# Optimization experiments

Measured on AMD Instinct MI355X. Metric: run time of the kernel, lower is better.

The kernel has to match this reference:

```python
import jax, jax.numpy as jnp
import numpy as np

EPS = 1e-8  # matches torch F.cosine_similarity eps


def setup_inputs() -> dict:
    key = jax.random.key(0)
    k1, k2, k3 = jax.random.split(key, 3)
    S, B, H = 16, 512, 2048
    OGLogits = jax.random.normal(k1, (B, H), dtype=jnp.float32)
    enhancedSamplesLogits = jax.random.normal(k2, (S, B, H), dtype=jnp.float32)
    W = jax.random.normal(k3, (H, H), dtype=jnp.float32) * (1.0 / np.sqrt(H))
    b = jnp.zeros((H,), dtype=jnp.float32)
    return {"OGLogits": OGLogits, "enhancedSamplesLogits": enhancedSamplesLogits, "W": W, "b": b}


def reference(OGLogits, enhancedSamplesLogits, W, b):
    # Original torch code builds the full (S*B, B) cosine-similarity matrix and
    # keeps only the diagonal via an eye mask; mathematically that equals the
    # per-pair cosine similarity cos(enhanced[s,b], OG[b]), computed directly here.
    e_norm = jnp.linalg.norm(enhancedSamplesLogits, axis=-1)          # (S, B)
    o_norm = jnp.linalg.norm(OGLogits, axis=-1)                       # (B,)
    dots = jnp.einsum('sbh,bh->sb', enhancedSamplesLogits, OGLogits)  # (S, B)
    sims = dots / jnp.maximum(e_norm * o_norm[None, :], EPS)          # (S, B)
    weighted = enhancedSamplesLogits * sims[..., None]                # (S, B, H)
    weightedRep = weighted.mean(axis=0)                               # (B, H)
    return weightedRep @ W.T + b                                      # (B, H)
```

## Files before the change

### kernel.cpp

```cpp
#include <hip/hip_runtime.h>

#define S_DIM 16
#define B_DIM 512
#define H_DIM 2048
#define EPS 1e-8f

typedef short bf16x8 __attribute__((ext_vector_type(8)));
typedef float f32x4 __attribute__((ext_vector_type(4)));

__device__ __forceinline__ unsigned short f2bf(float f) {
    union { float f; unsigned int u; } v; v.f = f;
    unsigned int u = v.u;
    unsigned int r = (u + 0x7fffu + ((u >> 16) & 1u)) >> 16;
    return (unsigned short)r;
}

__device__ __forceinline__ float dot4(const float4& a, const float4& b) {
    return a.x*b.x + a.y*b.y + a.z*b.z + a.w*b.w;
}

__global__ __launch_bounds__(512, 4) void simwrep_kernel(
    const float* __restrict__ OG, const float* __restrict__ E,
    const float* __restrict__ W, unsigned short* __restrict__ wrep,
    unsigned short* __restrict__ Wb) {
    const int b = blockIdx.x;
    const int t = threadIdx.x;
    const int lane = t & 63;
    const int wave = t >> 6;

    __shared__ float4 ogs[512];
    __shared__ float4 buf[8][512];
    __shared__ float red[8];

    const float4* og4 = (const float4*)(OG + (size_t)b * H_DIM);
    float4 o = og4[t];
    ogs[t] = o;
    float p = dot4(o, o);
    #pragma unroll
    for (int m = 32; m >= 1; m >>= 1) p += __shfl_xor(p, m, 64);
    if (lane == 0) red[wave] = p;
    __syncthreads();
    float og2 = 0.f;
    #pragma unroll
    for (int w = 0; w < 8; ++w) og2 += red[w];
    const float onorm = sqrtf(og2);

    const float4* e4a = (const float4*)(E + ((size_t)wave * B_DIM + b) * H_DIM);
    const float4* e4b = (const float4*)(E + ((size_t)(wave + 8) * B_DIM + b) * H_DIM);
    float4 ea[8], eb[8];
    #pragma unroll
    for (int i = 0; i < 8; ++i) {
        ea[i] = e4a[i * 64 + lane];
        eb[i] = e4b[i * 64 + lane];
    }
    float da = 0.f, na = 0.f, db = 0.f, nb = 0.f;
    #pragma unroll
    for (int i = 0; i < 8; ++i) {
        float4 og = ogs[i * 64 + lane];
        da += dot4(ea[i], og);
        na += dot4(ea[i], ea[i]);
        db += dot4(eb[i], og);
        nb += dot4(eb[i], eb[i]);
    }
    #pragma unroll
    for (int m = 32; m >= 1; m >>= 1) {
        da += __shfl_xor(da, m, 64);
        na += __shfl_xor(na, m, 64);
        db += __shfl_xor(db, m, 64);
        nb += __shfl_xor(nb, m, 64);
    }
    const float sima = da / fmaxf(sqrtf(na) * onorm, EPS);
    const float simb = db / fmaxf(sqrtf(nb) * onorm, EPS);

    #pragma unroll
    for (int i = 0; i < 8; ++i) {
        float4 v;
        v.x = ea[i].x * sima + eb[i].x * simb;
        v.y = ea[i].y * sima + eb[i].y * simb;
        v.z = ea[i].z * sima + eb[i].z * simb;
        v.w = ea[i].w * sima + eb[i].w * simb;
        buf[wave][i * 64 + lane] = v;
    }
    __syncthreads();

    float4 s = buf[0][t];
    #pragma unroll
    for (int w = 1; w < 8; ++w) {
        float4 v = buf[w][t];
        s.x += v.x; s.y += v.y; s.z += v.z; s.w += v.w;
    }
    const float sc = 1.f / (float)S_DIM;
    ushort4 ob;
    ob.x = f2bf(s.x * sc); ob.y = f2bf(s.y * sc);
    ob.z = f2bf(s.z * sc); ob.w = f2bf(s.w * sc);
    ((ushort4*)wrep)[(size_t)b * (H_DIM / 4) + t] = ob;

    const float4* w4 = (const float4*)W;
    #pragma unroll
    for (int j = 0; j < 4; ++j) {
        const size_t idx = (size_t)b * 2048 + j * 512 + t;
        float4 v = w4[idx];
        ushort4 c;
        c.x = f2bf(v.x); c.y = f2bf(v.y); c.z = f2bf(v.z); c.w = f2bf(v.w);
        ((ushort4*)Wb)[idx] = c;
    }
}

__global__ __launch_bounds__(256) void gemm_kernel(
    const unsigned short* __restrict__ A, const unsigned short* __restrict__ Wb,
    const float* __restrict__ bias, float* __restrict__ out) {
    const int n0 = blockIdx.x * 32;
    const int m0 = blockIdx.y * 64;

    __shared__ unsigned short As[2][64][72];
    __shared__ unsigned short Ws[2][32][72];

    const int t = threadIdx.x;
    const int lane = t & 63;
    const int wave = t >> 6;
    const int wm = (wave & 1) * 32;
    const int wn = (wave >> 1) * 16;

    const int lrA = t >> 2, lqA = t & 3;
    const int lrB = t >> 3, lqB = t & 7;

    const unsigned short* ap = A + (size_t)(m0 + lrA) * H_DIM + lqA * 16;
    const unsigned short* bp = Wb + (size_t)(n0 + lrB) * H_DIM + lqB * 8;

    f32x4 acc0 = {0.f, 0.f, 0.f, 0.f};
    f32x4 acc1 = {0.f, 0.f, 0.f, 0.f};

    const int row = lane & 15;
    const int q = lane >> 4;

    uint4 av0 = *(const uint4*)(ap);
    uint4 av1 = *(const uint4*)(ap + 8);
    uint4 bv  = *(const uint4*)(bp);
    *(uint4*)&As[0][lrA][lqA * 16]     = av0;
    *(uint4*)&As[0][lrA][lqA * 16 + 8] = av1;
    *(uint4*)&Ws[0][lrB][lqB * 8]      = bv;
    __syncthreads();

    for (int ki = 0; ki < 32; ++ki) {
        const int cur = ki & 1, nxt = cur ^ 1;
        if (ki + 1 < 32) {
            av0 = *(const uint4*)(ap + (ki + 1) * 64);
            av1 = *(const uint4*)(ap + (ki + 1) * 64 + 8);
            bv  = *(const uint4*)(bp + (ki + 1) * 64);
        }
        #pragma unroll
        for (int ks = 0; ks < 2; ++ks) {
            bf16x8 a0 = *(const bf16x8*)&As[cur][wm + row][ks * 32 + q * 8];
            bf16x8 a1 = *(const bf16x8*)&As[cur][wm + 16 + row][ks * 32 + q * 8];
            bf16x8 b0 = *(const bf16x8*)&Ws[cur][wn + row][ks * 32 + q * 8];
            acc0 = __builtin_amdgcn_mfma_f32_16x16x32_bf16(a0, b0, acc0, 0, 0, 0);
            acc1 = __builtin_amdgcn_mfma_f32_16x16x32_bf16(a1, b0, acc1, 0, 0, 0);
        }
        if (ki + 1 < 32) {
            *(uint4*)&As[nxt][lrA][lqA * 16]     = av0;
            *(uint4*)&As[nxt][lrA][lqA * 16 + 8] = av1;
            *(uint4*)&Ws[nxt][lrB][lqB * 8]      = bv;
        }
        __syncthreads();
    }

    const int col = lane & 15;
    const float bias0 = bias[n0 + wn + col];
    #pragma unroll
    for (int r = 0; r < 4; ++r) {
        const int mr = q * 4 + r;
        float* o0 = out + (size_t)(m0 + wm + mr) * H_DIM + n0 + wn;
        float* o1 = out + (size_t)(m0 + wm + 16 + mr) * H_DIM + n0 + wn;
        o0[col] = acc0[r] + bias0;
        o1[col] = acc1[r] + bias0;
    }
}

extern "C" void kernel_launch(void* const* d_in, const int* in_sizes, int n_in,
                              void* d_out, int out_size, void* d_ws, size_t ws_size,
                              hipStream_t stream) {
    const float* OG   = (const float*)d_in[0];
    const float* E    = (const float*)d_in[1];
    const float* W    = (const float*)d_in[2];
    const float* bias = (const float*)d_in[3];
    float* out = (float*)d_out;

    unsigned short* wrep = (unsigned short*)d_ws;
    unsigned short* Wb   = wrep + (size_t)B_DIM * H_DIM;

    simwrep_kernel<<<B_DIM, 512, 0, stream>>>(OG, E, W, wrep, Wb);
    gemm_kernel<<<dim3(H_DIM / 32, B_DIM / 64), 256, 0, stream>>>(wrep, Wb, bias, out);
}
```

Measured before the change: 126.3 us.

## Split similarity and weighted mean into separate kernels; use 32x32 MFMA tiles in GEMM

The fused per-batch kernel is split in two. One kernel computes the cosine similarity of each (s,b) row with one wave per row, and extra blocks in the same launch convert W to bf16. A second kernel re-reads E to form the weighted mean. The GEMM moves from a 64x32 tile built on 16x16x32 MFMAs to a 64x64 tile built on 32x32x16 MFMAs, which improves operand reuse and halves the grid. The price is reading E, about 64 MB, twice plus one extra kernel launch, in exchange for more parallelism in the similarity stage.

```diff
diff --git a/kernel.cpp b/kernel.cpp
--- a/kernel.cpp
+++ b/kernel.cpp
@@ -6,7 +6,7 @@
 #define EPS 1e-8f
 
 typedef short bf16x8 __attribute__((ext_vector_type(8)));
-typedef float f32x4 __attribute__((ext_vector_type(4)));
+typedef float f32x16 __attribute__((ext_vector_type(16)));
 
 __device__ __forceinline__ unsigned short f2bf(float f) {
     union { float f; unsigned int u; } v; v.f = f;
@@ -19,160 +19,138 @@
     return a.x*b.x + a.y*b.y + a.z*b.z + a.w*b.w;
 }
 
-__global__ __launch_bounds__(512, 4) void simwrep_kernel(
+__global__ __launch_bounds__(256) void sims_kernel(
     const float* __restrict__ OG, const float* __restrict__ E,
-    const float* __restrict__ W, unsigned short* __restrict__ wrep,
+    const float* __restrict__ W, float* __restrict__ sims,
     unsigned short* __restrict__ Wb) {
+    const int bid = blockIdx.x;
+    if (bid < (S_DIM * B_DIM / 4)) {
+        const int lane = threadIdx.x & 63;
+        const int r = bid * 4 + (threadIdx.x >> 6);
+        const int b = r & (B_DIM - 1);
+        const float4* e4  = (const float4*)E  + (size_t)r * (H_DIM / 4);
+        const float4* og4 = (const float4*)OG + (size_t)b * (H_DIM / 4);
+        float d = 0.f, n = 0.f, o = 0.f;
+        #pragma unroll
+        for (int i = 0; i < 8; ++i) {
+            float4 e = e4[i * 64 + lane];
+            float4 g = og4[i * 64 + lane];
+            d += dot4(e, g); n += dot4(e, e); o += dot4(g, g);
+        }
+        #pragma unroll
+        for (int m = 32; m >= 1; m >>= 1) {
+            d += __shfl_xor(d, m, 64);
+            n += __shfl_xor(n, m, 64);
+            o += __shfl_xor(o, m, 64);
+        }
+        if (lane == 0) sims[r] = d / fmaxf(sqrtf(n) * sqrtf(o), EPS);
+    } else {
+        const int wb = bid - (S_DIM * B_DIM / 4);
+        const int t = threadIdx.x;
+        const float4* w4 = (const float4*)W;
+        ushort4* wb4 = (ushort4*)Wb;
+        #pragma unroll
+        for (int j = 0; j < 8; ++j) {
+            const size_t idx = (size_t)wb * 2048 + j * 256 + t;
+            float4 v = w4[idx];
+            ushort4 c;
+            c.x = f2bf(v.x); c.y = f2bf(v.y); c.z = f2bf(v.z); c.w = f2bf(v.w);
+            wb4[idx] = c;
+        }
+    }
+}
+
+__global__ __launch_bounds__(512) void wmean_kernel(
+    const float* __restrict__ E, const float* __restrict__ sims,
+    unsigned short* __restrict__ wrep) {
     const int b = blockIdx.x;
     const int t = threadIdx.x;
-    const int lane = t & 63;
-    const int wave = t >> 6;
-
-    __shared__ float4 ogs[512];
-    __shared__ float4 buf[8][512];
-    __shared__ float red[8];
-
-    const float4* og4 = (const float4*)(OG + (size_t)b * H_DIM);
-    float4 o = og4[t];
-    ogs[t] = o;
-    float p = dot4(o, o);
+    __shared__ float sl[S_DIM];
+    const float4* e4 = (const float4*)E;
+    float4 ev[S_DIM];
     #pragma unroll
-    for (int m = 32; m >= 1; m >>= 1) p += __shfl_xor(p, m, 64);
-    if (lane == 0) red[wave] = p;
+    for (int s = 0; s < S_DIM; ++s)
+        ev[s] = e4[((size_t)s * B_DIM + b) * (H_DIM / 4) + t];
+    if (t < S_DIM) sl[t] = sims[t * B_DIM + b];
     __syncthreads();
-    float og2 = 0.f;
+    float x = 0.f, y = 0.f, z = 0.f, w = 0.f;
     #pragma unroll
-    for (int w = 0; w < 8; ++w) og2 += red[w];
-    const float onorm = sqrtf(og2);
-
-    const float4* e4a = (const float4*)(E + ((size_t)wave * B_DIM + b) * H_DIM);
-    const float4* e4b = (const float4*)(E + ((size_t)(wave + 8) * B_DIM + b) * H_DIM);
-    float4 ea[8], eb[8];
-    #pragma unroll
-    for (int i = 0; i < 8; ++i) {
-        ea[i] = e4a[i * 64 + lane];
-        eb[i] = e4b[i * 64 + lane];
-    }
-    float da = 0.f, na = 0.f, db = 0.f, nb = 0.f;
-    #pragma unroll
-    for (int i = 0; i < 8; ++i) {
-        float4 og = ogs[i * 64 + lane];
-        da += dot4(ea[i], og);
-        na += dot4(ea[i], ea[i]);
-        db += dot4(eb[i], og);
-        nb += dot4(eb[i], eb[i]);
-    }
-    #pragma unroll
-    for (int m = 32; m >= 1; m >>= 1) {
-        da += __shfl_xor(da, m, 64);
-        na += __shfl_xor(na, m, 64);
-        db += __shfl_xor(db, m, 64);
-        nb += __shfl_xor(nb, m, 64);
-    }
-    const float sima = da / fmaxf(sqrtf(na) * onorm, EPS);
-    const float simb = db / fmaxf(sqrtf(nb) * onorm, EPS);
-
-    #pragma unroll
-    for (int i = 0; i < 8; ++i) {
-        float4 v;
-        v.x = ea[i].x * sima + eb[i].x * simb;
-        v.y = ea[i].y * sima + eb[i].y * simb;
-        v.z = ea[i].z * sima + eb[i].z * simb;
-        v.w = ea[i].w * sima + eb[i].w * simb;
-        buf[wave][i * 64 + lane] = v;
-    }
-    __syncthreads();
-
-    float4 s = buf[0][t];
-    #pragma unroll
-    for (int w = 1; w < 8; ++w) {
-        float4 v = buf[w][t];
-        s.x += v.x; s.y += v.y; s.z += v.z; s.w += v.w;
+    for (int s = 0; s < S_DIM; ++s) {
+        const float sm = sl[s];
+        x += sm * ev[s].x; y += sm * ev[s].y;
+        z += sm * ev[s].z; w += sm * ev[s].w;
     }
     const float sc = 1.f / (float)S_DIM;
     ushort4 ob;
-    ob.x = f2bf(s.x * sc); ob.y = f2bf(s.y * sc);
-    ob.z = f2bf(s.z * sc); ob.w = f2bf(s.w * sc);
+    ob.x = f2bf(x * sc); ob.y = f2bf(y * sc);
+    ob.z = f2bf(z * sc); ob.w = f2bf(w * sc);
     ((ushort4*)wrep)[(size_t)b * (H_DIM / 4) + t] = ob;
-
-    const float4* w4 = (const float4*)W;
-    #pragma unroll
-    for (int j = 0; j < 4; ++j) {
-        const size_t idx = (size_t)b * 2048 + j * 512 + t;
-        float4 v = w4[idx];
-        ushort4 c;
-        c.x = f2bf(v.x); c.y = f2bf(v.y); c.z = f2bf(v.z); c.w = f2bf(v.w);
-        ((ushort4*)Wb)[idx] = c;
-    }
 }
 
 __global__ __launch_bounds__(256) void gemm_kernel(
     const unsigned short* __restrict__ A, const unsigned short* __restrict__ Wb,
     const float* __restrict__ bias, float* __restrict__ out) {
-    const int n0 = blockIdx.x * 32;
+    const int n0 = blockIdx.x * 64;
     const int m0 = blockIdx.y * 64;
 
     __shared__ unsigned short As[2][64][72];
-    __shared__ unsigned short Ws[2][32][72];
+    __shared__ unsigned short Bs[2][64][72];
 
     const int t = threadIdx.x;
     const int lane = t & 63;
     const int wave = t >> 6;
     const int wm = (wave & 1) * 32;
-    const int wn = (wave >> 1) * 16;
+    const int wn = (wave >> 1) * 32;
 
-    const int lrA = t >> 2, lqA = t & 3;
-    const int lrB = t >> 3, lqB = t & 7;
+    const int lr = t >> 2, lq = t & 3;
+    const unsigned short* ap = A  + (size_t)(m0 + lr) * H_DIM + lq * 16;
+    const unsigned short* bp = Wb + (size_t)(n0 + lr) * H_DIM + lq * 16;
 
-    const unsigned short* ap = A + (size_t)(m0 + lrA) * H_DIM + lqA * 16;
-    const unsigned short* bp = Wb + (size_t)(n0 + lrB) * H_DIM + lqB * 8;
+    f32x16 acc = {0.f,0.f,0.f,0.f,0.f,0.f,0.f,0.f,
+                  0.f,0.f,0.f,0.f,0.f,0.f,0.f,0.f};
 
-    f32x4 acc0 = {0.f, 0.f, 0.f, 0.f};
-    f32x4 acc1 = {0.f, 0.f, 0.f, 0.f};
+    const int row = lane & 31;
+    const int hi = lane >> 5;
 
-    const int row = lane & 15;
-    const int q = lane >> 4;
-
-    uint4 av0 = *(const uint4*)(ap);
-    uint4 av1 = *(const uint4*)(ap + 8);
-    uint4 bv  = *(const uint4*)(bp);
-    *(uint4*)&As[0][lrA][lqA * 16]     = av0;
-    *(uint4*)&As[0][lrA][lqA * 16 + 8] = av1;
-    *(uint4*)&Ws[0][lrB][lqB * 8]      = bv;
+    uint4 a0 = *(const uint4*)(ap);
+    uint4 a1 = *(const uint4*)(ap + 8);
+    uint4 b0 = *(const uint4*)(bp);
+    uint4 b1 = *(const uint4*)(bp + 8);
+    *(uint4*)&As[0][lr][lq * 16]     = a0;
+    *(uint4*)&As[0][lr][lq * 16 + 8] = a1;
+    *(uint4*)&Bs[0][lr][lq * 16]     = b0;
+    *(uint4*)&Bs[0][lr][lq * 16 + 8] = b1;
     __syncthreads();
 
     for (int ki = 0; ki < 32; ++ki) {
         const int cur = ki & 1, nxt = cur ^ 1;
         if (ki + 1 < 32) {
-            av0 = *(const uint4*)(ap + (ki + 1) * 64);
-            av1 = *(const uint4*)(ap + (ki + 1) * 64 + 8);
-            bv  = *(const uint4*)(bp + (ki + 1) * 64);
+            a0 = *(const uint4*)(ap + (ki + 1) * 64);
+            a1 = *(const uint4*)(ap + (ki + 1) * 64 + 8);
+            b0 = *(const uint4*)(bp + (ki + 1) * 64);
+            b1 = *(const uint4*)(bp + (ki + 1) * 64 + 8);
         }
         #pragma unroll
-        for (int ks = 0; ks < 2; ++ks) {
-            bf16x8 a0 = *(const bf16x8*)&As[cur][wm + row][ks * 32 + q * 8];
-            bf16x8 a1 = *(const bf16x8*)&As[cur][wm + 16 + row][ks * 32 + q * 8];
-            bf16x8 b0 = *(const bf16x8*)&Ws[cur][wn + row][ks * 32 + q * 8];
-            acc0 = __builtin_amdgcn_mfma_f32_16x16x32_bf16(a0, b0, acc0, 0, 0, 0);
-            acc1 = __builtin_amdgcn_mfma_f32_16x16x32_bf16(a1, b0, acc1, 0, 0, 0);
+        for (int ks = 0; ks < 4; ++ks) {
+            bf16x8 af  = *(const bf16x8*)&As[cur][wm + row][ks * 16 + hi * 8];
+            bf16x8 bfr = *(const bf16x8*)&Bs[cur][wn + row][ks * 16 + hi * 8];
+            acc = __builtin_amdgcn_mfma_f32_32x32x16_bf16(af, bfr, acc, 0, 0, 0);
         }
         if (ki + 1 < 32) {
-            *(uint4*)&As[nxt][lrA][lqA * 16]     = av0;
-            *(uint4*)&As[nxt][lrA][lqA * 16 + 8] = av1;
-            *(uint4*)&Ws[nxt][lrB][lqB * 8]      = bv;
+            *(uint4*)&As[nxt][lr][lq * 16]     = a0;
+            *(uint4*)&As[nxt][lr][lq * 16 + 8] = a1;
+            *(uint4*)&Bs[nxt][lr][lq * 16]     = b0;
+            *(uint4*)&Bs[nxt][lr][lq * 16 + 8] = b1;
         }
         __syncthreads();
     }
 
-    const int col = lane & 15;
+    const int col = lane & 31;
     const float bias0 = bias[n0 + wn + col];
     #pragma unroll
-    for (int r = 0; r < 4; ++r) {
-        const int mr = q * 4 + r;
-        float* o0 = out + (size_t)(m0 + wm + mr) * H_DIM + n0 + wn;
-        float* o1 = out + (size_t)(m0 + wm + 16 + mr) * H_DIM + n0 + wn;
-        o0[col] = acc0[r] + bias0;
-        o1[col] = acc1[r] + bias0;
+    for (int r = 0; r < 16; ++r) {
+        const int mr = (r & 3) + 8 * (r >> 2) + 4 * hi;
+        out[(size_t)(m0 + wm + mr) * H_DIM + n0 + wn + col] = acc[r] + bias0;
     }
 }
 
@@ -187,7 +165,9 @@
 
     unsigned short* wrep = (unsigned short*)d_ws;
     unsigned short* Wb   = wrep + (size_t)B_DIM * H_DIM;
+    float* sims          = (float*)(Wb + (size_t)H_DIM * H_DIM);
 
-    simwrep_kernel<<<B_DIM, 512, 0, stream>>>(OG, E, W, wrep, Wb);
-    gemm_kernel<<<dim3(H_DIM / 32, B_DIM / 64), 256, 0, stream>>>(wrep, Wb, bias, out);
+    sims_kernel<<<(S_DIM * B_DIM / 4) + 512, 256, 0, stream>>>(OG, E, W, sims, Wb);
+    wmean_kernel<<<B_DIM, 512, 0, stream>>>(E, sims, wrep);
+    gemm_kernel<<<dim3(H_DIM / 64, B_DIM / 64), 256, 0, stream>>>(wrep, Wb, bias, out);
 }
```

New measurement: 141.3 us. 1.12x slower.
